# Kernel optimization log

Hardware: AMD Instinct MI355X
Metric: run time of the kernel (lower is better)

## Reference

```python
import jax, jax.numpy as jnp
import numpy as np

B, T, E, H = 2, 256, 512, 8
D = E // H  # head_dim = 64 (even)


def setup_inputs() -> dict:
    key = jax.random.key(0)
    ks = jax.random.split(key, 4)
    x = jax.random.normal(ks[0], (B, T, E), jnp.float32)
    # pairwise complex rotary mask, stored as (..., 2) = (real, imag)
    attn_mask = jax.random.normal(ks[1], (B, 1, T, T, D // 2, 2), jnp.float32)
    pad_mask = jnp.zeros((B, 1, 1, T), jnp.float32)
    Wqkv = jax.random.normal(ks[2], (E, 3 * E), jnp.float32) * (E ** -0.5)
    bqkv = jnp.zeros((3 * E,), jnp.float32)
    Wo = jax.random.normal(ks[3], (E, E), jnp.float32) * (E ** -0.5)
    bo = jnp.zeros((E,), jnp.float32)
    return {"x": x, "attn_mask": attn_mask, "pad_mask": pad_mask,
            "Wqkv": Wqkv, "bqkv": bqkv, "Wo": Wo, "bo": bo}


def reference(x, attn_mask, pad_mask, Wqkv, bqkv, Wo, bo):
    scale = 1.0 / np.sqrt(D)
    qkv = x @ Wqkv + bqkv                                   # (B,T,3E)
    q, k, v = jnp.split(qkv, 3, axis=-1)
    q = q.reshape(B, T, H, D).transpose(0, 2, 1, 3)         # (B,H,T,D)
    v = v.reshape(B, T, H, D).transpose(0, 2, 1, 3)         # (B,H,S,D)
    # keys as complex pairs: (B,H,1,S,D/2,2)
    k = k.reshape(B, T, H, D // 2, 2).transpose(0, 2, 1, 3, 4)[:, :, None]
    m = attn_mask                                           # (B,1,T,S,D/2,2)
    # complex multiply k * m -> rotated keys per (query, key) pair
    kr = k[..., 0] * m[..., 0] - k[..., 1] * m[..., 1]      # (B,H,T,S,D/2)
    ki = k[..., 0] * m[..., 1] + k[..., 1] * m[..., 0]
    krot = jnp.stack([kr, ki], axis=-1).reshape(B, H, T, T, D)
    a = jnp.einsum('bhtd,bhtsd->bhts', q, krot) * scale     # (B,H,T,S)
    a = a + pad_mask
    a = jax.nn.softmax(a, axis=-1)
    # (eval mode: no dropout)
    o = jnp.einsum('bhts,bhsd->bhtd', a, v)                 # (B,H,T,D)
    o = o.transpose(0, 2, 1, 3).reshape(B, T, E)
    o = o @ Wo + bo
    attn_weights = a.sum(axis=1) / H                        # (B,T,S)
    return o, attn_weights
```

## Files before the change

kernel.cpp:

```cpp
#include <hip/hip_runtime.h>
#include <math.h>

#define Bb 2
#define Tt 256
#define Ee 512
#define Hh 8
#define Dd 64
#define E3 1536
#define SCP 260

typedef float vfloat4 __attribute__((ext_vector_type(4)));
typedef short bf16x8 __attribute__((ext_vector_type(8)));
typedef float f32x4 __attribute__((ext_vector_type(4)));

__device__ inline float4 ntload4(const float* p) {
    vfloat4 v = __builtin_nontemporal_load((const vfloat4*)p);
    return make_float4(v.x, v.y, v.z, v.w);
}
template<int CTRL>
__device__ inline float dpp_addf(float v) {
    int x = __builtin_amdgcn_update_dpp(0, __float_as_int(v), CTRL, 0xF, 0xF, true);
    return v + __int_as_float(x);
}
__device__ inline float swz4_addf(float v) {
    int x = __builtin_amdgcn_ds_swizzle(__float_as_int(v), 0x101F);
    return v + __int_as_float(x);
}
__device__ inline unsigned short bf16rne(float f) {
    unsigned u = __float_as_uint(f);
    return (unsigned short)((u + 0x7FFFu + ((u >> 16) & 1u)) >> 16);
}
__device__ inline float bf16tof(unsigned short h) {
    return __uint_as_float(((unsigned)h) << 16);
}
__device__ inline bf16x8 ldb(const unsigned short* p) {
    return *(const bf16x8*)(const void*)p;
}
__device__ __forceinline__ void split8(const float* p, bf16x8& hi, bf16x8& lo) {
    const float4 a = *(const float4*)p, b = *(const float4*)(p + 4);
    float f[8] = {a.x, a.y, a.z, a.w, b.x, b.y, b.z, b.w};
    bf16x8 h, l;
    #pragma unroll
    for (int i = 0; i < 8; ++i) {
        const unsigned short hh = bf16rne(f[i]);
        h[i] = (short)hh;
        l[i] = (short)bf16rne(f[i] - bf16tof(hh));
    }
    hi = h; lo = l;
}
__device__ __forceinline__ void split8a(const float* f, bf16x8& hi, bf16x8& lo) {
    bf16x8 h, l;
    #pragma unroll
    for (int i = 0; i < 8; ++i) {
        const unsigned short hh = bf16rne(f[i]);
        h[i] = (short)hh;
        l[i] = (short)bf16rne(f[i] - bf16tof(hh));
    }
    hi = h; lo = l;
}
__device__ __forceinline__ f32x4 mfma3(f32x4 acc, bf16x8 ah, bf16x8 al,
                                       bf16x8 bh, bf16x8 bl) {
    acc = __builtin_amdgcn_mfma_f32_16x16x32_bf16(ah, bh, acc, 0, 0, 0);
    acc = __builtin_amdgcn_mfma_f32_16x16x32_bf16(al, bh, acc, 0, 0, 0);
    acc = __builtin_amdgcn_mfma_f32_16x16x32_bf16(ah, bl, acc, 0, 0, 0);
    return acc;
}

__global__ __launch_bounds__(256) void mfma_qkv2(
    const float* __restrict__ x, const float* __restrict__ Wqkv,
    const float* __restrict__ bias, float* __restrict__ C,
    const float* __restrict__ Wo,
    unsigned short* __restrict__ Wohi, unsigned short* __restrict__ Wolo)
{
    const int bid = blockIdx.x;
    const int tid = threadIdx.x;

    if (bid >= 768) {
        __shared__ float tile[64][65];
        const int b2 = bid - 768;
        const int kt = b2 & 7, nt = b2 >> 3;
        const int rr = tid >> 2, cc = (tid & 3) * 16;
        #pragma unroll
        for (int j = 0; j < 4; ++j) {
            const float4 v = *(const float4*)&Wo[(size_t)(kt * 64 + rr) * 512 + nt * 64 + cc + j * 4];
            tile[rr][cc + j * 4 + 0] = v.x;
            tile[rr][cc + j * 4 + 1] = v.y;
            tile[rr][cc + j * 4 + 2] = v.z;
            tile[rr][cc + j * 4 + 3] = v.w;
        }
        __syncthreads();
        unsigned short hb[16], lb[16];
        #pragma unroll
        for (int j = 0; j < 16; ++j) {
            const float f = tile[cc + j][rr];
            const unsigned short h = bf16rne(f);
            hb[j] = h;
            lb[j] = bf16rne(f - bf16tof(h));
        }
        const size_t off = (size_t)(nt * 64 + rr) * 512 + kt * 64 + cc;
        *(uint4*)&Wohi[off]     = *(const uint4*)&hb[0];
        *(uint4*)&Wohi[off + 8] = *(const uint4*)&hb[8];
        *(uint4*)&Wolo[off]     = *(const uint4*)&lb[0];
        *(uint4*)&Wolo[off + 8] = *(const uint4*)&lb[8];
        return;
    }

    __shared__ f32x4 red[4][2][2][64];
    const int lane = tid & 63;
    const int wv   = tid >> 6;
    const int n0   = (bid % 48) * 32;
    const int m0   = (bid / 48) * 32;
    const int fr   = lane & 15;
    const int kg   = (lane >> 4) * 8;

    f32x4 acc00 = {0.f, 0.f, 0.f, 0.f}, acc01 = acc00, acc10 = acc00, acc11 = acc00;

    #pragma unroll
    for (int s = 0; s < 4; ++s) {
        const int k0 = wv * 128 + s * 32 + kg;
        bf16x8 ah0, al0, ah1, al1;
        split8(&x[(size_t)(m0 + fr) * 512 + k0], ah0, al0);
        split8(&x[(size_t)(m0 + 16 + fr) * 512 + k0], ah1, al1);
        float b0[8], b1[8];
        #pragma unroll
        for (int j = 0; j < 8; ++j) {
            b0[j] = Wqkv[(size_t)(k0 + j) * E3 + n0 + fr];
            b1[j] = Wqkv[(size_t)(k0 + j) * E3 + n0 + 16 + fr];
        }
        bf16x8 bh0, bl0, bh1, bl1;
        split8a(b0, bh0, bl0);
        split8a(b1, bh1, bl1);
        acc00 = mfma3(acc00, ah0, al0, bh0, bl0);
        acc01 = mfma3(acc01, ah0, al0, bh1, bl1);
        acc10 = mfma3(acc10, ah1, al1, bh0, bl0);
        acc11 = mfma3(acc11, ah1, al1, bh1, bl1);
    }
    red[wv][0][0][lane] = acc00;
    red[wv][0][1][lane] = acc01;
    red[wv][1][0][lane] = acc10;
    red[wv][1][1][lane] = acc11;
    __syncthreads();

    const int fi = wv >> 1, fj = wv & 1;
    f32x4 s0 = red[0][fi][fj][lane];
    const f32x4 s1 = red[1][fi][fj][lane];
    const f32x4 s2 = red[2][fi][fj][lane];
    const f32x4 s3 = red[3][fi][fj][lane];
    #pragma unroll
    for (int g = 0; g < 4; ++g) s0[g] = (s0[g] + s1[g]) + (s2[g] + s3[g]);
    const int dr = (lane >> 4) * 4, dc = lane & 15;
    const float bs = bias[n0 + fj * 16 + dc];
    #pragma unroll
    for (int g = 0; g < 4; ++g)
        C[(size_t)(m0 + fi * 16 + dr + g) * E3 + n0 + fj * 16 + dc] = s0[g] + bs;
}

__global__ __launch_bounds__(256) void mfma_proj(
    const unsigned short* __restrict__ Ahi, const unsigned short* __restrict__ Alo,
    const unsigned short* __restrict__ Bhi, const unsigned short* __restrict__ Blo,
    const float* __restrict__ bias, float* __restrict__ C, int M, int N)
{
    __shared__ f32x4 red[4][2][2][64];
    const int lane = threadIdx.x & 63;
    const int wv   = threadIdx.x >> 6;
    const int m0   = blockIdx.y * 32;
    const int n0   = blockIdx.x * 32;
    const int fr   = lane & 15;
    const int kg   = (lane >> 4) * 8;

    f32x4 acc00 = {0.f, 0.f, 0.f, 0.f}, acc01 = acc00, acc10 = acc00, acc11 = acc00;

    #pragma unroll
    for (int s = 0; s < 4; ++s) {
        const int k0 = wv * 128 + s * 32 + kg;
        const bf16x8 ah0 = ldb(Ahi + (size_t)(m0 + fr) * 512 + k0);
        const bf16x8 al0 = ldb(Alo + (size_t)(m0 + fr) * 512 + k0);
        const bf16x8 ah1 = ldb(Ahi + (size_t)(m0 + 16 + fr) * 512 + k0);
        const bf16x8 al1 = ldb(Alo + (size_t)(m0 + 16 + fr) * 512 + k0);
        const bf16x8 bh0 = ldb(Bhi + (size_t)(n0 + fr) * 512 + k0);
        const bf16x8 bl0 = ldb(Blo + (size_t)(n0 + fr) * 512 + k0);
        const bf16x8 bh1 = ldb(Bhi + (size_t)(n0 + 16 + fr) * 512 + k0);
        const bf16x8 bl1 = ldb(Blo + (size_t)(n0 + 16 + fr) * 512 + k0);
        acc00 = mfma3(acc00, ah0, al0, bh0, bl0);
        acc01 = mfma3(acc01, ah0, al0, bh1, bl1);
        acc10 = mfma3(acc10, ah1, al1, bh0, bl0);
        acc11 = mfma3(acc11, ah1, al1, bh1, bl1);
    }
    red[wv][0][0][lane] = acc00;
    red[wv][0][1][lane] = acc01;
    red[wv][1][0][lane] = acc10;
    red[wv][1][1][lane] = acc11;
    __syncthreads();

    const int fi = wv >> 1, fj = wv & 1;
    f32x4 s0 = red[0][fi][fj][lane];
    const f32x4 s1 = red[1][fi][fj][lane];
    const f32x4 s2 = red[2][fi][fj][lane];
    const f32x4 s3 = red[3][fi][fj][lane];
    #pragma unroll
    for (int g = 0; g < 4; ++g) s0[g] = (s0[g] + s1[g]) + (s2[g] + s3[g]);
    const int dr = (lane >> 4) * 4, dc = lane & 15;
    const float bs = bias[n0 + fj * 16 + dc];
    #pragma unroll
    for (int g = 0; g < 4; ++g)
        C[(size_t)(m0 + fi * 16 + dr + g) * N + n0 + fj * 16 + dc] = s0[g] + bs;
}

__global__ __launch_bounds__(512, 2) void attn_kernel(
    const float* __restrict__ qkv, const float* __restrict__ mask,
    const float* __restrict__ pad,
    unsigned short* __restrict__ oahi, unsigned short* __restrict__ oalo,
    float* __restrict__ attn_w)
{
    __shared__ float sc[2][Hh][SCP];
    __shared__ float part[4][2][Hh][68];
    __shared__ float rrs[16];
    const int tid  = threadIdx.x;
    const int lane = tid & 63;
    const int wv   = tid >> 6;
    const int si   = lane >> 3;
    const int dq   = lane & 7;
    const int b    = blockIdx.x >> 7;
    const int t0   = (blockIdx.x & 127) * 2;

    float4 qr[2][Hh][2];
    {
        const float* qb = qkv + (size_t)(b * Tt + t0) * E3 + dq * 8;
        #pragma unroll
        for (int t = 0; t < 2; ++t)
            #pragma unroll
            for (int h = 0; h < Hh; ++h) {
                qr[t][h][0] = *(const float4*)(qb + (size_t)t * E3 + h * 64);
                qr[t][h][1] = *(const float4*)(qb + (size_t)t * E3 + h * 64 + 4);
            }
    }
    const float scale = 0.125f;

    const float* mbase0 = mask + (size_t)(b * Tt + t0) * Tt * Dd + dq * 8;
    const float* mbase1 = mbase0 + (size_t)Tt * Dd;
    float4 mc[2][4];
    {
        const int s0 = wv * 32 + si;
        const float* m0p = mbase0 + (size_t)s0 * Dd;
        const float* m1p = mbase1 + (size_t)s0 * Dd;
        mc[0][0] = ntload4(m0p); mc[0][1] = ntload4(m0p + 4);
        mc[0][2] = ntload4(m1p); mc[0][3] = ntload4(m1p + 4);
    }
    #pragma unroll
    for (int c = 0; c < 4; ++c) {
        const int s = wv * 32 + c * 8 + si;
        const int cb = c & 1, nbm = cb ^ 1;
        if (c < 3) {
            const int sn = s + 8;
            const float* m0p = mbase0 + (size_t)sn * Dd;
            const float* m1p = mbase1 + (size_t)sn * Dd;
            mc[nbm][0] = ntload4(m0p); mc[nbm][1] = ntload4(m0p + 4);
            mc[nbm][2] = ntload4(m1p); mc[nbm][3] = ntload4(m1p + 4);
        }
        const float4 ma0 = mc[cb][0], mb0 = mc[cb][1];
        const float4 ma1 = mc[cb][2], mb1 = mc[cb][3];
        const float* krow = qkv + (size_t)(b * Tt + s) * E3 + Ee + dq * 8;
        const float padv = pad[b * Tt + s];
        float4 kc[2][2];
        kc[0][0] = *(const float4*)(krow);
        kc[0][1] = *(const float4*)(krow + 4);
        #pragma unroll
        for (int h = 0; h < Hh; ++h) {
            const int hb = h & 1, hn = hb ^ 1;
            if (h < 7) {
                kc[hn][0] = *(const float4*)(krow + (h + 1) * 64);
                kc[hn][1] = *(const float4*)(krow + (h + 1) * 64 + 4);
            }
            const float4 ka = kc[hb][0], kb = kc[hb][1];
            const float4 qa0 = qr[0][h][0], qb0 = qr[0][h][1];
            const float4 qa1 = qr[1][h][0], qb1 = qr[1][h][1];
            float u0 = qa0.x * ka.x + qa0.y * ka.y;
            float w0 = qa0.y * ka.x - qa0.x * ka.y;
            float u1 = qa0.z * ka.z + qa0.w * ka.w;
            float w1 = qa0.w * ka.z - qa0.z * ka.w;
            float u2 = qb0.x * kb.x + qb0.y * kb.y;
            float w2 = qb0.y * kb.x - qb0.x * kb.y;
            float u3 = qb0.z * kb.z + qb0.w * kb.w;
            float w3 = qb0.w * kb.z - qb0.z * kb.w;
            float v0 = u0 * ma0.x + w0 * ma0.y + u1 * ma0.z + w1 * ma0.w
                     + u2 * mb0.x + w2 * mb0.y + u3 * mb0.z + w3 * mb0.w;
            float s0 = qa1.x * ka.x + qa1.y * ka.y;
            float r0 = qa1.y * ka.x - qa1.x * ka.y;
            float s1 = qa1.z * ka.z + qa1.w * ka.w;
            float r1 = qa1.w * ka.z - qa1.z * ka.w;
            float s2 = qb1.x * kb.x + qb1.y * kb.y;
            float r2 = qb1.y * kb.x - qb1.x * kb.y;
            float s3 = qb1.z * kb.z + qb1.w * kb.w;
            float r3 = qb1.w * kb.z - qb1.z * kb.w;
            float v1 = s0 * ma1.x + r0 * ma1.y + s1 * ma1.z + r1 * ma1.w
                     + s2 * mb1.x + r2 * mb1.y + s3 * mb1.z + r3 * mb1.w;
            v0 = dpp_addf<0xB1>(v0); v0 = dpp_addf<0x4E>(v0); v0 = swz4_addf(v0);
            v1 = dpp_addf<0xB1>(v1); v1 = dpp_addf<0x4E>(v1); v1 = swz4_addf(v1);
            if (dq == 0) {
                sc[0][h][s] = v0 * scale + padv;
                sc[1][h][s] = v1 * scale + padv;
            }
        }
    }
    __syncthreads();

    #pragma unroll
    for (int r = 0; r < 2; ++r) {
        const int row = wv * 2 + r;
        float* pr = &sc[0][0][0] + row * SCP;
        float4 xv = *(const float4*)&pr[lane * 4];
        float mx = fmaxf(fmaxf(xv.x, xv.y), fmaxf(xv.z, xv.w));
        #pragma unroll
        for (int dlt = 32; dlt >= 1; dlt >>= 1) mx = fmaxf(mx, __shfl_xor(mx, dlt));
        float4 ev;
        ev.x = __expf(xv.x - mx);
        ev.y = __expf(xv.y - mx);
        ev.z = __expf(xv.z - mx);
        ev.w = __expf(xv.w - mx);
        float sum = (ev.x + ev.y) + (ev.z + ev.w);
        #pragma unroll
        for (int dlt = 32; dlt >= 1; dlt >>= 1) sum += __shfl_xor(sum, dlt);
        *(float4*)&pr[lane * 4] = ev;
        if (lane == 0) rrs[row] = 1.0f / sum;
    }
    __syncthreads();

    {
        const int tt = tid >> 8, s2 = tid & 255;
        float aw = 0.f;
        #pragma unroll
        for (int h = 0; h < Hh; ++h) aw += sc[tt][h][s2] * rrs[tt * 8 + h];
        attn_w[(size_t)(b * Tt + t0 + tt) * Tt + s2] = aw * 0.125f;
    }

    {
        const int sh = tid >> 7;
        const int h  = (tid >> 4) & 7;
        const int d4 = tid & 15;
        const float* vb = qkv + (size_t)b * Tt * E3 + 2 * Ee + h * 64 + d4 * 4;
        float4 o0 = make_float4(0.f, 0.f, 0.f, 0.f);
        float4 o1 = make_float4(0.f, 0.f, 0.f, 0.f);
        const int sBeg = sh * 64;
        float4 vc[2][4];
        #pragma unroll
        for (int i = 0; i < 4; ++i)
            vc[0][i] = *(const float4*)(vb + (size_t)(sBeg + i) * E3);
        #pragma unroll
        for (int it = 0; it < 16; ++it) {
            const int s2 = sBeg + it * 4;
            const int cb = it & 1, nbv = cb ^ 1;
            if (it < 15) {
                #pragma unroll
                for (int i = 0; i < 4; ++i)
                    vc[nbv][i] = *(const float4*)(vb + (size_t)(s2 + 4 + i) * E3);
            }
            const float4 p0 = *(const float4*)&sc[0][h][s2];
            const float4 p1 = *(const float4*)&sc[1][h][s2];
            const float4 va = vc[cb][0], vbv = vc[cb][1], vcv = vc[cb][2], vd = vc[cb][3];
            o0.x = fmaf(p0.x, va.x, o0.x);  o0.y = fmaf(p0.x, va.y, o0.y);
            o0.z = fmaf(p0.x, va.z, o0.z);  o0.w = fmaf(p0.x, va.w, o0.w);
            o0.x = fmaf(p0.y, vbv.x, o0.x); o0.y = fmaf(p0.y, vbv.y, o0.y);
            o0.z = fmaf(p0.y, vbv.z, o0.z); o0.w = fmaf(p0.y, vbv.w, o0.w);
            o0.x = fmaf(p0.z, vcv.x, o0.x); o0.y = fmaf(p0.z, vcv.y, o0.y);
            o0.z = fmaf(p0.z, vcv.z, o0.z); o0.w = fmaf(p0.z, vcv.w, o0.w);
            o0.x = fmaf(p0.w, vd.x, o0.x);  o0.y = fmaf(p0.w, vd.y, o0.y);
            o0.z = fmaf(p0.w, vd.z, o0.z);  o0.w = fmaf(p0.w, vd.w, o0.w);
            o1.x = fmaf(p1.x, va.x, o1.x);  o1.y = fmaf(p1.x, va.y, o1.y);
            o1.z = fmaf(p1.x, va.z, o1.z);  o1.w = fmaf(p1.x, va.w, o1.w);
            o1.x = fmaf(p1.y, vbv.x, o1.x); o1.y = fmaf(p1.y, vbv.y, o1.y);
            o1.z = fmaf(p1.y, vbv.z, o1.z); o1.w = fmaf(p1.y, vbv.w, o1.w);
            o1.x = fmaf(p1.z, vcv.x, o1.x); o1.y = fmaf(p1.z, vcv.y, o1.y);
            o1.z = fmaf(p1.z, vcv.z, o1.z); o1.w = fmaf(p1.z, vcv.w, o1.w);
            o1.x = fmaf(p1.w, vd.x, o1.x);  o1.y = fmaf(p1.w, vd.y, o1.y);
            o1.z = fmaf(p1.w, vd.z, o1.z);  o1.w = fmaf(p1.w, vd.w, o1.w);
        }
        *(float4*)&part[sh][0][h][d4 * 4] = o0;
        *(float4*)&part[sh][1][h][d4 * 4] = o1;
    }
    __syncthreads();

    {
        const int t  = tid >> 8;
        const int n2 = tid & 255;
        const int h  = n2 >> 5;
        const int dc = (2 * n2) & 63;
        const float rr = rrs[t * 8 + h];
        float ax = 0.f, ay = 0.f;
        #pragma unroll
        for (int s = 0; s < 4; ++s) {
            const float2 p = *(const float2*)&part[s][t][h][dc];
            ax += p.x; ay += p.y;
        }
        const float ox = ax * rr, oy = ay * rr;
        const unsigned short hx = bf16rne(ox), hy = bf16rne(oy);
        const unsigned short lx = bf16rne(ox - bf16tof(hx));
        const unsigned short ly = bf16rne(oy - bf16tof(hy));
        const size_t off = (size_t)(b * Tt + t0 + t) * Ee + 2 * n2;
        *(unsigned*)&oahi[off] = (unsigned)hx | ((unsigned)hy << 16);
        *(unsigned*)&oalo[off] = (unsigned)lx | ((unsigned)ly << 16);
    }
}

extern "C" void kernel_launch(void* const* d_in, const int* in_sizes, int n_in,
                              void* d_out, int out_size, void* d_ws, size_t ws_size,
                              hipStream_t stream) {
    const float* x    = (const float*)d_in[0];
    const float* mask = (const float*)d_in[1];
    const float* pad  = (const float*)d_in[2];
    const float* Wqkv = (const float*)d_in[3];
    const float* bqkv = (const float*)d_in[4];
    const float* Wo   = (const float*)d_in[5];
    const float* bo   = (const float*)d_in[6];

    float* out = (float*)d_out;

    unsigned short* Wohi = (unsigned short*)d_ws;
    unsigned short* Wolo = Wohi + 262144;
    unsigned short* oahi = Wolo + 262144;
    unsigned short* oalo = oahi + 262144;
    float* qkv = (float*)(oalo + 262144);

    mfma_qkv2<<<832, 256, 0, stream>>>(x, Wqkv, bqkv, qkv, Wo, Wohi, Wolo);

    attn_kernel<<<dim3(Bb * (Tt / 2)), 512, 0, stream>>>(
        qkv, mask, pad, oahi, oalo, out + (size_t)Bb * Tt * Ee);

    mfma_proj<<<dim3(Ee / 32, (Bb * Tt) / 32), 256, 0, stream>>>(
        oahi, oalo, Wohi, Wolo, bo, out, Bb * Tt, Ee);
}
```

Measured before the change: 46.65 us.

## Fuse QKV GEMM, attention and output projection into one cooperative kernel

Replaces the three kernel launches (QKV GEMM plus Wo conversion, attention, output projection) with a single cooperative kernel of 256 blocks of 512 threads. Grid-wide syncs separate the phases. Each block does three QKV tiles with an 8-wave K split and the attention for two query rows. The aim is to remove launch gaps and inter-kernel drain/fill time. In exchange it adds grid barrier costs, uses fewer blocks for the GEMM phases, and does a larger cross-wave reduction through shared memory.

```diff
diff --git a/kernel.cpp b/kernel.cpp
--- a/kernel.cpp
+++ b/kernel.cpp
@@ -1,5 +1,8 @@
 #include <hip/hip_runtime.h>
+#include <hip/hip_cooperative_groups.h>
 #include <math.h>
+
+namespace cg = cooperative_groups;
 
 #define Bb 2
 #define Tt 256
@@ -66,338 +69,351 @@
     return acc;
 }
 
-__global__ __launch_bounds__(256) void mfma_qkv2(
-    const float* __restrict__ x, const float* __restrict__ Wqkv,
-    const float* __restrict__ bias, float* __restrict__ C,
-    const float* __restrict__ Wo,
-    unsigned short* __restrict__ Wohi, unsigned short* __restrict__ Wolo)
+__global__ __launch_bounds__(512, 2) void fused_all(
+    const float* __restrict__ x, const float* __restrict__ mask,
+    const float* __restrict__ pad, const float* __restrict__ Wqkv,
+    const float* __restrict__ bqkv, const float* __restrict__ Wo,
+    const float* __restrict__ bo, float* __restrict__ out,
+    unsigned short* __restrict__ Wohi, unsigned short* __restrict__ Wolo,
+    unsigned short* __restrict__ oahi, unsigned short* __restrict__ oalo,
+    float* __restrict__ qkv)
 {
-    const int bid = blockIdx.x;
-    const int tid = threadIdx.x;
-
-    if (bid >= 768) {
-        __shared__ float tile[64][65];
-        const int b2 = bid - 768;
-        const int kt = b2 & 7, nt = b2 >> 3;
-        const int rr = tid >> 2, cc = (tid & 3) * 16;
-        #pragma unroll
-        for (int j = 0; j < 4; ++j) {
-            const float4 v = *(const float4*)&Wo[(size_t)(kt * 64 + rr) * 512 + nt * 64 + cc + j * 4];
-            tile[rr][cc + j * 4 + 0] = v.x;
-            tile[rr][cc + j * 4 + 1] = v.y;
-            tile[rr][cc + j * 4 + 2] = v.z;
-            tile[rr][cc + j * 4 + 3] = v.w;
-        }
-        __syncthreads();
-        unsigned short hb[16], lb[16];
-        #pragma unroll
-        for (int j = 0; j < 16; ++j) {
-            const float f = tile[cc + j][rr];
-            const unsigned short h = bf16rne(f);
-            hb[j] = h;
-            lb[j] = bf16rne(f - bf16tof(h));
-        }
-        const size_t off = (size_t)(nt * 64 + rr) * 512 + kt * 64 + cc;
-        *(uint4*)&Wohi[off]     = *(const uint4*)&hb[0];
-        *(uint4*)&Wohi[off + 8] = *(const uint4*)&hb[8];
-        *(uint4*)&Wolo[off]     = *(const uint4*)&lb[0];
-        *(uint4*)&Wolo[off + 8] = *(const uint4*)&lb[8];
-        return;
-    }
-
-    __shared__ f32x4 red[4][2][2][64];
-    const int lane = tid & 63;
-    const int wv   = tid >> 6;
-    const int n0   = (bid % 48) * 32;
-    const int m0   = (bid / 48) * 32;
-    const int fr   = lane & 15;
-    const int kg   = (lane >> 4) * 8;
-
-    f32x4 acc00 = {0.f, 0.f, 0.f, 0.f}, acc01 = acc00, acc10 = acc00, acc11 = acc00;
-
-    #pragma unroll
-    for (int s = 0; s < 4; ++s) {
-        const int k0 = wv * 128 + s * 32 + kg;
-        bf16x8 ah0, al0, ah1, al1;
-        split8(&x[(size_t)(m0 + fr) * 512 + k0], ah0, al0);
-        split8(&x[(size_t)(m0 + 16 + fr) * 512 + k0], ah1, al1);
-        float b0[8], b1[8];
-        #pragma unroll
-        for (int j = 0; j < 8; ++j) {
-            b0[j] = Wqkv[(size_t)(k0 + j) * E3 + n0 + fr];
-            b1[j] = Wqkv[(size_t)(k0 + j) * E3 + n0 + 16 + fr];
-        }
-        bf16x8 bh0, bl0, bh1, bl1;
-        split8a(b0, bh0, bl0);
-        split8a(b1, bh1, bl1);
-        acc00 = mfma3(acc00, ah0, al0, bh0, bl0);
-        acc01 = mfma3(acc01, ah0, al0, bh1, bl1);
-        acc10 = mfma3(acc10, ah1, al1, bh0, bl0);
-        acc11 = mfma3(acc11, ah1, al1, bh1, bl1);
-    }
-    red[wv][0][0][lane] = acc00;
-    red[wv][0][1][lane] = acc01;
-    red[wv][1][0][lane] = acc10;
-    red[wv][1][1][lane] = acc11;
-    __syncthreads();
-
-    const int fi = wv >> 1, fj = wv & 1;
-    f32x4 s0 = red[0][fi][fj][lane];
-    const f32x4 s1 = red[1][fi][fj][lane];
-    const f32x4 s2 = red[2][fi][fj][lane];
-    const f32x4 s3 = red[3][fi][fj][lane];
-    #pragma unroll
-    for (int g = 0; g < 4; ++g) s0[g] = (s0[g] + s1[g]) + (s2[g] + s3[g]);
-    const int dr = (lane >> 4) * 4, dc = lane & 15;
-    const float bs = bias[n0 + fj * 16 + dc];
-    #pragma unroll
-    for (int g = 0; g < 4; ++g)
-        C[(size_t)(m0 + fi * 16 + dr + g) * E3 + n0 + fj * 16 + dc] = s0[g] + bs;
-}
-
-__global__ __launch_bounds__(256) void mfma_proj(
-    const unsigned short* __restrict__ Ahi, const unsigned short* __restrict__ Alo,
-    const unsigned short* __restrict__ Bhi, const unsigned short* __restrict__ Blo,
-    const float* __restrict__ bias, float* __restrict__ C, int M, int N)
-{
-    __shared__ f32x4 red[4][2][2][64];
-    const int lane = threadIdx.x & 63;
-    const int wv   = threadIdx.x >> 6;
-    const int m0   = blockIdx.y * 32;
-    const int n0   = blockIdx.x * 32;
-    const int fr   = lane & 15;
-    const int kg   = (lane >> 4) * 8;
-
-    f32x4 acc00 = {0.f, 0.f, 0.f, 0.f}, acc01 = acc00, acc10 = acc00, acc11 = acc00;
-
-    #pragma unroll
-    for (int s = 0; s < 4; ++s) {
-        const int k0 = wv * 128 + s * 32 + kg;
-        const bf16x8 ah0 = ldb(Ahi + (size_t)(m0 + fr) * 512 + k0);
-        const bf16x8 al0 = ldb(Alo + (size_t)(m0 + fr) * 512 + k0);
-        const bf16x8 ah1 = ldb(Ahi + (size_t)(m0 + 16 + fr) * 512 + k0);
-        const bf16x8 al1 = ldb(Alo + (size_t)(m0 + 16 + fr) * 512 + k0);
-        const bf16x8 bh0 = ldb(Bhi + (size_t)(n0 + fr) * 512 + k0);
-        const bf16x8 bl0 = ldb(Blo + (size_t)(n0 + fr) * 512 + k0);
-        const bf16x8 bh1 = ldb(Bhi + (size_t)(n0 + 16 + fr) * 512 + k0);
-        const bf16x8 bl1 = ldb(Blo + (size_t)(n0 + 16 + fr) * 512 + k0);
-        acc00 = mfma3(acc00, ah0, al0, bh0, bl0);
-        acc01 = mfma3(acc01, ah0, al0, bh1, bl1);
-        acc10 = mfma3(acc10, ah1, al1, bh0, bl0);
-        acc11 = mfma3(acc11, ah1, al1, bh1, bl1);
-    }
-    red[wv][0][0][lane] = acc00;
-    red[wv][0][1][lane] = acc01;
-    red[wv][1][0][lane] = acc10;
-    red[wv][1][1][lane] = acc11;
-    __syncthreads();
-
-    const int fi = wv >> 1, fj = wv & 1;
-    f32x4 s0 = red[0][fi][fj][lane];
-    const f32x4 s1 = red[1][fi][fj][lane];
-    const f32x4 s2 = red[2][fi][fj][lane];
-    const f32x4 s3 = red[3][fi][fj][lane];
-    #pragma unroll
-    for (int g = 0; g < 4; ++g) s0[g] = (s0[g] + s1[g]) + (s2[g] + s3[g]);
-    const int dr = (lane >> 4) * 4, dc = lane & 15;
-    const float bs = bias[n0 + fj * 16 + dc];
-    #pragma unroll
-    for (int g = 0; g < 4; ++g)
-        C[(size_t)(m0 + fi * 16 + dr + g) * N + n0 + fj * 16 + dc] = s0[g] + bs;
-}
-
-__global__ __launch_bounds__(512, 2) void attn_kernel(
-    const float* __restrict__ qkv, const float* __restrict__ mask,
-    const float* __restrict__ pad,
-    unsigned short* __restrict__ oahi, unsigned short* __restrict__ oalo,
-    float* __restrict__ attn_w)
-{
-    __shared__ float sc[2][Hh][SCP];
-    __shared__ float part[4][2][Hh][68];
-    __shared__ float rrs[16];
+    cg::grid_group grid = cg::this_grid();
+    __shared__ __align__(16) char smem[34816];
+
+    const int bid  = blockIdx.x;
     const int tid  = threadIdx.x;
     const int lane = tid & 63;
     const int wv   = tid >> 6;
-    const int si   = lane >> 3;
-    const int dq   = lane & 7;
-    const int b    = blockIdx.x >> 7;
-    const int t0   = (blockIdx.x & 127) * 2;
-
-    float4 qr[2][Hh][2];
+
+    float* attn_w = out + (size_t)Bb * Tt * Ee;
+
     {
-        const float* qb = qkv + (size_t)(b * Tt + t0) * E3 + dq * 8;
+        float (*tile)[65] = (float(*)[65])smem;
+        const bool act = (bid < 64) && (tid < 256);
+        const int kt = bid & 7, nt = bid >> 3;
+        const int rr = (tid & 255) >> 2, cc = (tid & 3) * 16;
+        if (act) {
+            #pragma unroll
+            for (int j = 0; j < 4; ++j) {
+                const float4 v = *(const float4*)&Wo[(size_t)(kt * 64 + rr) * 512 + nt * 64 + cc + j * 4];
+                tile[rr][cc + j * 4 + 0] = v.x;
+                tile[rr][cc + j * 4 + 1] = v.y;
+                tile[rr][cc + j * 4 + 2] = v.z;
+                tile[rr][cc + j * 4 + 3] = v.w;
+            }
+        }
+        __syncthreads();
+        if (act) {
+            unsigned short hb[16], lb[16];
+            #pragma unroll
+            for (int j = 0; j < 16; ++j) {
+                const float f = tile[cc + j][rr];
+                const unsigned short h = bf16rne(f);
+                hb[j] = h;
+                lb[j] = bf16rne(f - bf16tof(h));
+            }
+            const size_t off = (size_t)(nt * 64 + rr) * 512 + kt * 64 + cc;
+            *(uint4*)&Wohi[off]     = *(const uint4*)&hb[0];
+            *(uint4*)&Wohi[off + 8] = *(const uint4*)&hb[8];
+            *(uint4*)&Wolo[off]     = *(const uint4*)&lb[0];
+            *(uint4*)&Wolo[off + 8] = *(const uint4*)&lb[8];
+        }
+    }
+    __syncthreads();
+
+    {
+        f32x4 (*red)[2][2][64] = (f32x4(*)[2][2][64])smem;
+        const int fr = lane & 15;
+        const int kg = (lane >> 4) * 8;
         #pragma unroll
-        for (int t = 0; t < 2; ++t)
+        for (int uu = 0; uu < 3; ++uu) {
+            const int unit = bid * 3 + uu;
+            const int n0 = (unit % 48) * 32;
+            const int m0 = (unit / 48) * 32;
+            f32x4 acc00 = {0.f, 0.f, 0.f, 0.f}, acc01 = acc00, acc10 = acc00, acc11 = acc00;
+            #pragma unroll
+            for (int s = 0; s < 2; ++s) {
+                const int k0 = wv * 64 + s * 32 + kg;
+                bf16x8 ah0, al0, ah1, al1;
+                split8(&x[(size_t)(m0 + fr) * 512 + k0], ah0, al0);
+                split8(&x[(size_t)(m0 + 16 + fr) * 512 + k0], ah1, al1);
+                float b0[8], b1[8];
+                #pragma unroll
+                for (int j = 0; j < 8; ++j) {
+                    b0[j] = Wqkv[(size_t)(k0 + j) * E3 + n0 + fr];
+                    b1[j] = Wqkv[(size_t)(k0 + j) * E3 + n0 + 16 + fr];
+                }
+                bf16x8 bh0, bl0, bh1, bl1;
+                split8a(b0, bh0, bl0);
+                split8a(b1, bh1, bl1);
+                acc00 = mfma3(acc00, ah0, al0, bh0, bl0);
+                acc01 = mfma3(acc01, ah0, al0, bh1, bl1);
+                acc10 = mfma3(acc10, ah1, al1, bh0, bl0);
+                acc11 = mfma3(acc11, ah1, al1, bh1, bl1);
+            }
+            red[wv][0][0][lane] = acc00;
+            red[wv][0][1][lane] = acc01;
+            red[wv][1][0][lane] = acc10;
+            red[wv][1][1][lane] = acc11;
+            __syncthreads();
+            if (wv < 4) {
+                const int fi = wv >> 1, fj = wv & 1;
+                f32x4 t = red[0][fi][fj][lane];
+                #pragma unroll
+                for (int r = 1; r < 8; ++r) {
+                    const f32x4 u = red[r][fi][fj][lane];
+                    #pragma unroll
+                    for (int g = 0; g < 4; ++g) t[g] += u[g];
+                }
+                const int dr = (lane >> 4) * 4, dc = lane & 15;
+                const float bs = bqkv[n0 + fj * 16 + dc];
+                #pragma unroll
+                for (int g = 0; g < 4; ++g)
+                    qkv[(size_t)(m0 + fi * 16 + dr + g) * E3 + n0 + fj * 16 + dc] = t[g] + bs;
+            }
+            __syncthreads();
+        }
+    }
+
+    grid.sync();
+
+    {
+        typedef float ScT[Hh][SCP];
+        ScT* sc = (ScT*)smem;
+        typedef float PartT[2][Hh][68];
+        PartT* part = (PartT*)(smem + 16640);
+        float* rrs = (float*)(smem + 16640 + 17408);
+
+        const int si = lane >> 3;
+        const int dq = lane & 7;
+        const int b  = bid >> 7;
+        const int t0 = (bid & 127) * 2;
+
+        float4 qr[2][Hh][2];
+        {
+            const float* qb = qkv + (size_t)(b * Tt + t0) * E3 + dq * 8;
+            #pragma unroll
+            for (int t = 0; t < 2; ++t)
+                #pragma unroll
+                for (int h = 0; h < Hh; ++h) {
+                    qr[t][h][0] = *(const float4*)(qb + (size_t)t * E3 + h * 64);
+                    qr[t][h][1] = *(const float4*)(qb + (size_t)t * E3 + h * 64 + 4);
+                }
+        }
+        const float scale = 0.125f;
+
+        const float* mbase0 = mask + (size_t)(b * Tt + t0) * Tt * Dd + dq * 8;
+        const float* mbase1 = mbase0 + (size_t)Tt * Dd;
+        float4 mc[2][4];
+        {
+            const int s0 = wv * 32 + si;
+            const float* m0p = mbase0 + (size_t)s0 * Dd;
+            const float* m1p = mbase1 + (size_t)s0 * Dd;
+            mc[0][0] = ntload4(m0p); mc[0][1] = ntload4(m0p + 4);
+            mc[0][2] = ntload4(m1p); mc[0][3] = ntload4(m1p + 4);
+        }
+        #pragma unroll
+        for (int c = 0; c < 4; ++c) {
+            const int s = wv * 32 + c * 8 + si;
+            const int cb = c & 1, nbm = cb ^ 1;
+            if (c < 3) {
+                const int sn = s + 8;
+                const float* m0p = mbase0 + (size_t)sn * Dd;
+                const float* m1p = mbase1 + (size_t)sn * Dd;
+                mc[nbm][0] = ntload4(m0p); mc[nbm][1] = ntload4(m0p + 4);
+                mc[nbm][2] = ntload4(m1p); mc[nbm][3] = ntload4(m1p + 4);
+            }
+            const float4 ma0 = mc[cb][0], mb0 = mc[cb][1];
+            const float4 ma1 = mc[cb][2], mb1 = mc[cb][3];
+            const float* krow = qkv + (size_t)(b * Tt + s) * E3 + Ee + dq * 8;
+            const float padv = pad[b * Tt + s];
+            float4 kc[2][2];
+            kc[0][0] = *(const float4*)(krow);
+            kc[0][1] = *(const float4*)(krow + 4);
             #pragma unroll
             for (int h = 0; h < Hh; ++h) {
-                qr[t][h][0] = *(const float4*)(qb + (size_t)t * E3 + h * 64);
-                qr[t][h][1] = *(const float4*)(qb + (size_t)t * E3 + h * 64 + 4);
-            }
-    }
-    const float scale = 0.125f;
-
-    const float* mbase0 = mask + (size_t)(b * Tt + t0) * Tt * Dd + dq * 8;
-    const float* mbase1 = mbase0 + (size_t)Tt * Dd;
-    float4 mc[2][4];
+                const int hb = h & 1, hn = hb ^ 1;
+                if (h < 7) {
+                    kc[hn][0] = *(const float4*)(krow + (h + 1) * 64);
+                    kc[hn][1] = *(const float4*)(krow + (h + 1) * 64 + 4);
+                }
+                const float4 ka = kc[hb][0], kb = kc[hb][1];
+                const float4 qa0 = qr[0][h][0], qb0 = qr[0][h][1];
+                const float4 qa1 = qr[1][h][0], qb1 = qr[1][h][1];
+                float u0 = qa0.x * ka.x + qa0.y * ka.y;
+                float w0 = qa0.y * ka.x - qa0.x * ka.y;
+                float u1 = qa0.z * ka.z + qa0.w * ka.w;
+                float w1 = qa0.w * ka.z - qa0.z * ka.w;
+                float u2 = qb0.x * kb.x + qb0.y * kb.y;
+                float w2 = qb0.y * kb.x - qb0.x * kb.y;
+                float u3 = qb0.z * kb.z + qb0.w * kb.w;
+                float w3 = qb0.w * kb.z - qb0.z * kb.w;
+                float v0 = u0 * ma0.x + w0 * ma0.y + u1 * ma0.z + w1 * ma0.w
+                         + u2 * mb0.x + w2 * mb0.y + u3 * mb0.z + w3 * mb0.w;
+                float s0 = qa1.x * ka.x + qa1.y * ka.y;
+                float r0 = qa1.y * ka.x - qa1.x * ka.y;
+                float s1 = qa1.z * ka.z + qa1.w * ka.w;
+                float r1 = qa1.w * ka.z - qa1.z * ka.w;
+                float s2 = qb1.x * kb.x + qb1.y * kb.y;
+                float r2 = qb1.y * kb.x - qb1.x * kb.y;
+                float s3 = qb1.z * kb.z + qb1.w * kb.w;
+                float r3 = qb1.w * kb.z - qb1.z * kb.w;
+                float v1 = s0 * ma1.x + r0 * ma1.y + s1 * ma1.z + r1 * ma1.w
+                         + s2 * mb1.x + r2 * mb1.y + s3 * mb1.z + r3 * mb1.w;
+                v0 = dpp_addf<0xB1>(v0); v0 = dpp_addf<0x4E>(v0); v0 = swz4_addf(v0);
+                v1 = dpp_addf<0xB1>(v1); v1 = dpp_addf<0x4E>(v1); v1 = swz4_addf(v1);
+                if (dq == 0) {
+                    sc[0][h][s] = v0 * scale + padv;
+                    sc[1][h][s] = v1 * scale + padv;
+                }
+            }
+        }
+        __syncthreads();
+
+        #pragma unroll
+        for (int r = 0; r < 2; ++r) {
+            const int row = wv * 2 + r;
+            float* pr = &sc[0][0][0] + row * SCP;
+            float4 xv = *(const float4*)&pr[lane * 4];
+            float mx = fmaxf(fmaxf(xv.x, xv.y), fmaxf(xv.z, xv.w));
+            #pragma unroll
+            for (int dlt = 32; dlt >= 1; dlt >>= 1) mx = fmaxf(mx, __shfl_xor(mx, dlt));
+            float4 ev;
+            ev.x = __expf(xv.x - mx);
+            ev.y = __expf(xv.y - mx);
+            ev.z = __expf(xv.z - mx);
+            ev.w = __expf(xv.w - mx);
+            float sum = (ev.x + ev.y) + (ev.z + ev.w);
+            #pragma unroll
+            for (int dlt = 32; dlt >= 1; dlt >>= 1) sum += __shfl_xor(sum, dlt);
+            *(float4*)&pr[lane * 4] = ev;
+            if (lane == 0) rrs[row] = 1.0f / sum;
+        }
+        __syncthreads();
+
+        {
+            const int tt = tid >> 8, s2 = tid & 255;
+            float aw = 0.f;
+            #pragma unroll
+            for (int h = 0; h < Hh; ++h) aw += sc[tt][h][s2] * rrs[tt * 8 + h];
+            attn_w[(size_t)(b * Tt + t0 + tt) * Tt + s2] = aw * 0.125f;
+        }
+
+        {
+            const int sh = tid >> 7;
+            const int h  = (tid >> 4) & 7;
+            const int d4 = tid & 15;
+            const float* vb = qkv + (size_t)b * Tt * E3 + 2 * Ee + h * 64 + d4 * 4;
+            float4 o0 = make_float4(0.f, 0.f, 0.f, 0.f);
+            float4 o1 = make_float4(0.f, 0.f, 0.f, 0.f);
+            const int sBeg = sh * 64;
+            float4 vc[2][4];
+            #pragma unroll
+            for (int i = 0; i < 4; ++i)
+                vc[0][i] = *(const float4*)(vb + (size_t)(sBeg + i) * E3);
+            #pragma unroll
+            for (int it = 0; it < 16; ++it) {
+                const int s2 = sBeg + it * 4;
+                const int cb = it & 1, nbv = cb ^ 1;
+                if (it < 15) {
+                    #pragma unroll
+                    for (int i = 0; i < 4; ++i)
+                        vc[nbv][i] = *(const float4*)(vb + (size_t)(s2 + 4 + i) * E3);
+                }
+                const float4 p0 = *(const float4*)&sc[0][h][s2];
+                const float4 p1 = *(const float4*)&sc[1][h][s2];
+                const float4 va = vc[cb][0], vbv = vc[cb][1], vcv = vc[cb][2], vd = vc[cb][3];
+                o0.x = fmaf(p0.x, va.x, o0.x);  o0.y = fmaf(p0.x, va.y, o0.y);
+                o0.z = fmaf(p0.x, va.z, o0.z);  o0.w = fmaf(p0.x, va.w, o0.w);
+                o0.x = fmaf(p0.y, vbv.x, o0.x); o0.y = fmaf(p0.y, vbv.y, o0.y);
+                o0.z = fmaf(p0.y, vbv.z, o0.z); o0.w = fmaf(p0.y, vbv.w, o0.w);
+                o0.x = fmaf(p0.z, vcv.x, o0.x); o0.y = fmaf(p0.z, vcv.y, o0.y);
+                o0.z = fmaf(p0.z, vcv.z, o0.z); o0.w = fmaf(p0.z, vcv.w, o0.w);
+                o0.x = fmaf(p0.w, vd.x, o0.x);  o0.y = fmaf(p0.w, vd.y, o0.y);
+                o0.z = fmaf(p0.w, vd.z, o0.z);  o0.w = fmaf(p0.w, vd.w, o0.w);
+                o1.x = fmaf(p1.x, va.x, o1.x);  o1.y = fmaf(p1.x, va.y, o1.y);
+                o1.z = fmaf(p1.x, va.z, o1.z);  o1.w = fmaf(p1.x, va.w, o1.w);
+                o1.x = fmaf(p1.y, vbv.x, o1.x); o1.y = fmaf(p1.y, vbv.y, o1.y);
+                o1.z = fmaf(p1.y, vbv.z, o1.z); o1.w = fmaf(p1.y, vbv.w, o1.w);
+                o1.x = fmaf(p1.z, vcv.x, o1.x); o1.y = fmaf(p1.z, vcv.y, o1.y);
+                o1.z = fmaf(p1.z, vcv.z, o1.z); o1.w = fmaf(p1.z, vcv.w, o1.w);
+                o1.x = fmaf(p1.w, vd.x, o1.x);  o1.y = fmaf(p1.w, vd.y, o1.y);
+                o1.z = fmaf(p1.w, vd.z, o1.z);  o1.w = fmaf(p1.w, vd.w, o1.w);
+            }
+            *(float4*)&part[sh][0][h][d4 * 4] = o0;
+            *(float4*)&part[sh][1][h][d4 * 4] = o1;
+        }
+        __syncthreads();
+
+        {
+            const int t  = tid >> 8;
+            const int n2 = tid & 255;
+            const int h  = n2 >> 5;
+            const int dc = (2 * n2) & 63;
+            const float rr = rrs[t * 8 + h];
+            float ax = 0.f, ay = 0.f;
+            #pragma unroll
+            for (int s = 0; s < 4; ++s) {
+                const float2 p = *(const float2*)&part[s][t][h][dc];
+                ax += p.x; ay += p.y;
+            }
+            const float ox = ax * rr, oy = ay * rr;
+            const unsigned short hx = bf16rne(ox), hy = bf16rne(oy);
+            const unsigned short lx = bf16rne(ox - bf16tof(hx));
+            const unsigned short ly = bf16rne(oy - bf16tof(hy));
+            const size_t off = (size_t)(b * Tt + t0 + t) * Ee + 2 * n2;
+            *(unsigned*)&oahi[off] = (unsigned)hx | ((unsigned)hy << 16);
+            *(unsigned*)&oalo[off] = (unsigned)lx | ((unsigned)ly << 16);
+        }
+    }
+
+    grid.sync();
+
     {
-        const int s0 = wv * 32 + si;
-        const float* m0p = mbase0 + (size_t)s0 * Dd;
-        const float* m1p = mbase1 + (size_t)s0 * Dd;
-        mc[0][0] = ntload4(m0p); mc[0][1] = ntload4(m0p + 4);
-        mc[0][2] = ntload4(m1p); mc[0][3] = ntload4(m1p + 4);
-    }
-    #pragma unroll
-    for (int c = 0; c < 4; ++c) {
-        const int s = wv * 32 + c * 8 + si;
-        const int cb = c & 1, nbm = cb ^ 1;
-        if (c < 3) {
-            const int sn = s + 8;
-            const float* m0p = mbase0 + (size_t)sn * Dd;
-            const float* m1p = mbase1 + (size_t)sn * Dd;
-            mc[nbm][0] = ntload4(m0p); mc[nbm][1] = ntload4(m0p + 4);
-            mc[nbm][2] = ntload4(m1p); mc[nbm][3] = ntload4(m1p + 4);
-        }
-        const float4 ma0 = mc[cb][0], mb0 = mc[cb][1];
-        const float4 ma1 = mc[cb][2], mb1 = mc[cb][3];
-        const float* krow = qkv + (size_t)(b * Tt + s) * E3 + Ee + dq * 8;
-        const float padv = pad[b * Tt + s];
-        float4 kc[2][2];
-        kc[0][0] = *(const float4*)(krow);
-        kc[0][1] = *(const float4*)(krow + 4);
+        f32x4 (*red)[2][2][64] = (f32x4(*)[2][2][64])smem;
+        const int fr = lane & 15;
+        const int kg = (lane >> 4) * 8;
+        const int m0 = (bid >> 4) * 32;
+        const int n0 = (bid & 15) * 32;
+        f32x4 acc00 = {0.f, 0.f, 0.f, 0.f}, acc01 = acc00, acc10 = acc00, acc11 = acc00;
         #pragma unroll
-        for (int h = 0; h < Hh; ++h) {
-            const int hb = h & 1, hn = hb ^ 1;
-            if (h < 7) {
-                kc[hn][0] = *(const float4*)(krow + (h + 1) * 64);
-                kc[hn][1] = *(const float4*)(krow + (h + 1) * 64 + 4);
-            }
-            const float4 ka = kc[hb][0], kb = kc[hb][1];
-            const float4 qa0 = qr[0][h][0], qb0 = qr[0][h][1];
-            const float4 qa1 = qr[1][h][0], qb1 = qr[1][h][1];
-            float u0 = qa0.x * ka.x + qa0.y * ka.y;
-            float w0 = qa0.y * ka.x - qa0.x * ka.y;
-            float u1 = qa0.z * ka.z + qa0.w * ka.w;
-            float w1 = qa0.w * ka.z - qa0.z * ka.w;
-            float u2 = qb0.x * kb.x + qb0.y * kb.y;
-            float w2 = qb0.y * kb.x - qb0.x * kb.y;
-            float u3 = qb0.z * kb.z + qb0.w * kb.w;
-            float w3 = qb0.w * kb.z - qb0.z * kb.w;
-            float v0 = u0 * ma0.x + w0 * ma0.y + u1 * ma0.z + w1 * ma0.w
-                     + u2 * mb0.x + w2 * mb0.y + u3 * mb0.z + w3 * mb0.w;
-            float s0 = qa1.x * ka.x + qa1.y * ka.y;
-            float r0 = qa1.y * ka.x - qa1.x * ka.y;
-            float s1 = qa1.z * ka.z + qa1.w * ka.w;
-            float r1 = qa1.w * ka.z - qa1.z * ka.w;
-            float s2 = qb1.x * kb.x + qb1.y * kb.y;
-            float r2 = qb1.y * kb.x - qb1.x * kb.y;
-            float s3 = qb1.z * kb.z + qb1.w * kb.w;
-            float r3 = qb1.w * kb.z - qb1.z * kb.w;
-            float v1 = s0 * ma1.x + r0 * ma1.y + s1 * ma1.z + r1 * ma1.w
-                     + s2 * mb1.x + r2 * mb1.y + s3 * mb1.z + r3 * mb1.w;
-            v0 = dpp_addf<0xB1>(v0); v0 = dpp_addf<0x4E>(v0); v0 = swz4_addf(v0);
-            v1 = dpp_addf<0xB1>(v1); v1 = dpp_addf<0x4E>(v1); v1 = swz4_addf(v1);
-            if (dq == 0) {
-                sc[0][h][s] = v0 * scale + padv;
-                sc[1][h][s] = v1 * scale + padv;
-            }
-        }
-    }
-    __syncthreads();
-
-    #pragma unroll
-    for (int r = 0; r < 2; ++r) {
-        const int row = wv * 2 + r;
-        float* pr = &sc[0][0][0] + row * SCP;
-        float4 xv = *(const float4*)&pr[lane * 4];
-        float mx = fmaxf(fmaxf(xv.x, xv.y), fmaxf(xv.z, xv.w));
-        #pragma unroll
-        for (int dlt = 32; dlt >= 1; dlt >>= 1) mx = fmaxf(mx, __shfl_xor(mx, dlt));
-        float4 ev;
-        ev.x = __expf(xv.x - mx);
-        ev.y = __expf(xv.y - mx);
-        ev.z = __expf(xv.z - mx);
-        ev.w = __expf(xv.w - mx);
-        float sum = (ev.x + ev.y) + (ev.z + ev.w);
-        #pragma unroll
-        for (int dlt = 32; dlt >= 1; dlt >>= 1) sum += __shfl_xor(sum, dlt);
-        *(float4*)&pr[lane * 4] = ev;
-        if (lane == 0) rrs[row] = 1.0f / sum;
-    }
-    __syncthreads();
-
-    {
-        const int tt = tid >> 8, s2 = tid & 255;
-        float aw = 0.f;
-        #pragma unroll
-        for (int h = 0; h < Hh; ++h) aw += sc[tt][h][s2] * rrs[tt * 8 + h];
-        attn_w[(size_t)(b * Tt + t0 + tt) * Tt + s2] = aw * 0.125f;
-    }
-
-    {
-        const int sh = tid >> 7;
-        const int h  = (tid >> 4) & 7;
-        const int d4 = tid & 15;
-        const float* vb = qkv + (size_t)b * Tt * E3 + 2 * Ee + h * 64 + d4 * 4;
-        float4 o0 = make_float4(0.f, 0.f, 0.f, 0.f);
-        float4 o1 = make_float4(0.f, 0.f, 0.f, 0.f);
-        const int sBeg = sh * 64;
-        float4 vc[2][4];
-        #pragma unroll
-        for (int i = 0; i < 4; ++i)
-            vc[0][i] = *(const float4*)(vb + (size_t)(sBeg + i) * E3);
-        #pragma unroll
-        for (int it = 0; it < 16; ++it) {
-            const int s2 = sBeg + it * 4;
-            const int cb = it & 1, nbv = cb ^ 1;
-            if (it < 15) {
+        for (int s = 0; s < 2; ++s) {
+            const int k0 = wv * 64 + s * 32 + kg;
+            const bf16x8 ah0 = ldb(oahi + (size_t)(m0 + fr) * 512 + k0);
+            const bf16x8 al0 = ldb(oalo + (size_t)(m0 + fr) * 512 + k0);
+            const bf16x8 ah1 = ldb(oahi + (size_t)(m0 + 16 + fr) * 512 + k0);
+            const bf16x8 al1 = ldb(oalo + (size_t)(m0 + 16 + fr) * 512 + k0);
+            const bf16x8 bh0 = ldb(Wohi + (size_t)(n0 + fr) * 512 + k0);
+            const bf16x8 bl0 = ldb(Wolo + (size_t)(n0 + fr) * 512 + k0);
+            const bf16x8 bh1 = ldb(Wohi + (size_t)(n0 + 16 + fr) * 512 + k0);
+            const bf16x8 bl1 = ldb(Wolo + (size_t)(n0 + 16 + fr) * 512 + k0);
+            acc00 = mfma3(acc00, ah0, al0, bh0, bl0);
+            acc01 = mfma3(acc01, ah0, al0, bh1, bl1);
+            acc10 = mfma3(acc10, ah1, al1, bh0, bl0);
+            acc11 = mfma3(acc11, ah1, al1, bh1, bl1);
+        }
+        __syncthreads();
+        red[wv][0][0][lane] = acc00;
+        red[wv][0][1][lane] = acc01;
+        red[wv][1][0][lane] = acc10;
+        red[wv][1][1][lane] = acc11;
+        __syncthreads();
+        if (wv < 4) {
+            const int fi = wv >> 1, fj = wv & 1;
+            f32x4 t = red[0][fi][fj][lane];
+            #pragma unroll
+            for (int r = 1; r < 8; ++r) {
+                const f32x4 u = red[r][fi][fj][lane];
                 #pragma unroll
-                for (int i = 0; i < 4; ++i)
-                    vc[nbv][i] = *(const float4*)(vb + (size_t)(s2 + 4 + i) * E3);
-            }
-            const float4 p0 = *(const float4*)&sc[0][h][s2];
-            const float4 p1 = *(const float4*)&sc[1][h][s2];
-            const float4 va = vc[cb][0], vbv = vc[cb][1], vcv = vc[cb][2], vd = vc[cb][3];
-            o0.x = fmaf(p0.x, va.x, o0.x);  o0.y = fmaf(p0.x, va.y, o0.y);
-            o0.z = fmaf(p0.x, va.z, o0.z);  o0.w = fmaf(p0.x, va.w, o0.w);
-            o0.x = fmaf(p0.y, vbv.x, o0.x); o0.y = fmaf(p0.y, vbv.y, o0.y);
-            o0.z = fmaf(p0.y, vbv.z, o0.z); o0.w = fmaf(p0.y, vbv.w, o0.w);
-            o0.x = fmaf(p0.z, vcv.x, o0.x); o0.y = fmaf(p0.z, vcv.y, o0.y);
-            o0.z = fmaf(p0.z, vcv.z, o0.z); o0.w = fmaf(p0.z, vcv.w, o0.w);
-            o0.x = fmaf(p0.w, vd.x, o0.x);  o0.y = fmaf(p0.w, vd.y, o0.y);
-            o0.z = fmaf(p0.w, vd.z, o0.z);  o0.w = fmaf(p0.w, vd.w, o0.w);
-            o1.x = fmaf(p1.x, va.x, o1.x);  o1.y = fmaf(p1.x, va.y, o1.y);
-            o1.z = fmaf(p1.x, va.z, o1.z);  o1.w = fmaf(p1.x, va.w, o1.w);
-            o1.x = fmaf(p1.y, vbv.x, o1.x); o1.y = fmaf(p1.y, vbv.y, o1.y);
-            o1.z = fmaf(p1.y, vbv.z, o1.z); o1.w = fmaf(p1.y, vbv.w, o1.w);
-            o1.x = fmaf(p1.z, vcv.x, o1.x); o1.y = fmaf(p1.z, vcv.y, o1.y);
-            o1.z = fmaf(p1.z, vcv.z, o1.z); o1.w = fmaf(p1.z, vcv.w, o1.w);
-            o1.x = fmaf(p1.w, vd.x, o1.x);  o1.y = fmaf(p1.w, vd.y, o1.y);
-            o1.z = fmaf(p1.w, vd.z, o1.z);  o1.w = fmaf(p1.w, vd.w, o1.w);
-        }
-        *(float4*)&part[sh][0][h][d4 * 4] = o0;
-        *(float4*)&part[sh][1][h][d4 * 4] = o1;
-    }
-    __syncthreads();
-
-    {
-        const int t  = tid >> 8;
-        const int n2 = tid & 255;
-        const int h  = n2 >> 5;
-        const int dc = (2 * n2) & 63;
-        const float rr = rrs[t * 8 + h];
-        float ax = 0.f, ay = 0.f;
-        #pragma unroll
-        for (int s = 0; s < 4; ++s) {
-            const float2 p = *(const float2*)&part[s][t][h][dc];
-            ax += p.x; ay += p.y;
-        }
-        const float ox = ax * rr, oy = ay * rr;
-        const unsigned short hx = bf16rne(ox), hy = bf16rne(oy);
-        const unsigned short lx = bf16rne(ox - bf16tof(hx));
-        const unsigned short ly = bf16rne(oy - bf16tof(hy));
-        const size_t off = (size_t)(b * Tt + t0 + t) * Ee + 2 * n2;
-        *(unsigned*)&oahi[off] = (unsigned)hx | ((unsigned)hy << 16);
-        *(unsigned*)&oalo[off] = (unsigned)lx | ((unsigned)ly << 16);
+                for (int g = 0; g < 4; ++g) t[g] += u[g];
+            }
+            const int dr = (lane >> 4) * 4, dc = lane & 15;
+            const float bs = bo[n0 + fj * 16 + dc];
+            #pragma unroll
+            for (int g = 0; g < 4; ++g)
+                out[(size_t)(m0 + fi * 16 + dr + g) * Ee + n0 + fj * 16 + dc] = t[g] + bs;
+        }
     }
 }
 
@@ -420,11 +436,11 @@
     unsigned short* oalo = oahi + 262144;
     float* qkv = (float*)(oalo + 262144);
 
-    mfma_qkv2<<<832, 256, 0, stream>>>(x, Wqkv, bqkv, qkv, Wo, Wohi, Wolo);
-
-    attn_kernel<<<dim3(Bb * (Tt / 2)), 512, 0, stream>>>(
-        qkv, mask, pad, oahi, oalo, out + (size_t)Bb * Tt * Ee);
-
-    mfma_proj<<<dim3(Ee / 32, (Bb * Tt) / 32), 256, 0, stream>>>(
-        oahi, oalo, Wohi, Wolo, bo, out, Bb * Tt, Ee);
-}
+    void* args[] = {
+        (void*)&x, (void*)&mask, (void*)&pad, (void*)&Wqkv, (void*)&bqkv,
+        (void*)&Wo, (void*)&bo, (void*)&out,
+        (void*)&Wohi, (void*)&Wolo, (void*)&oahi, (void*)&oalo, (void*)&qkv
+    };
+    hipLaunchCooperativeKernel((void*)fused_all, dim3(256), dim3(512),
+                               args, 0, stream);
+}
```

Result: slower. 115.8 us (+148.3%).
